# Kernel tuning notes

Measured on AMD Instinct MI355X. Metric: run time of the kernel, lower is better.

The kernel has to match this reference:

```python
import jax, jax.numpy as jnp
import numpy as np

EMBED_DIM = 1024
NUM_HEADS = 16
HEAD_DIM = EMBED_DIM // NUM_HEADS
HIDDEN_DIM = 4096
EPS = 1e-5


def setup_inputs() -> dict:
    key = jax.random.key(0)
    ks = jax.random.split(key, 12)
    B, N, C, H = 4, 2048, EMBED_DIM, HIDDEN_DIM
    s = 0.02
    return {
        "x": jax.random.normal(ks[0], (B, N, C), jnp.float32),
        "ln1_g": jnp.ones((C,), jnp.float32),
        "ln1_b": jnp.zeros((C,), jnp.float32),
        "w_qkv": jax.random.normal(ks[1], (C, 3 * C), jnp.float32) * s,
        "w_proj": jax.random.normal(ks[2], (C, C), jnp.float32) * s,
        "b_proj": jnp.zeros((C,), jnp.float32),
        "ln2_g": jnp.ones((C,), jnp.float32),
        "ln2_b": jnp.zeros((C,), jnp.float32),
        "w1": jax.random.normal(ks[3], (C, H), jnp.float32) * s,
        "b1": jnp.zeros((H,), jnp.float32),
        "w2": jax.random.normal(ks[4], (H, C), jnp.float32) * s,
        "b2": jnp.zeros((C,), jnp.float32),
    }


def _layernorm(x, g, b):
    mu = jnp.mean(x, axis=-1, keepdims=True)
    var = jnp.mean(jnp.square(x - mu), axis=-1, keepdims=True)
    return (x - mu) * jax.lax.rsqrt(var + EPS) * g + b


def reference(x, ln1_g, ln1_b, w_qkv, w_proj, b_proj, ln2_g, ln2_b, w1, b1, w2, b2):
    B, N, C = x.shape
    # --- attention sub-block ---
    h = _layernorm(x, ln1_g, ln1_b)
    qkv = h @ w_qkv  # [B,N,3C]
    qkv = qkv.reshape(B, N, 3, NUM_HEADS, HEAD_DIM).transpose(2, 0, 3, 1, 4)
    q, k, v = qkv[0], qkv[1], qkv[2]  # each [B,H,N,D]
    scale = HEAD_DIM ** -0.5
    attn = jnp.einsum("bhqd,bhkd->bhqk", q, k) * scale  # materialized scores
    attn = jax.nn.softmax(attn, axis=-1)
    o = jnp.einsum("bhqk,bhkd->bhqd", attn, v)
    o = o.transpose(0, 2, 1, 3).reshape(B, N, C)
    x = x + (o @ w_proj + b_proj)
    # --- MLP sub-block ---
    h = _layernorm(x, ln2_g, ln2_b)
    h = jax.nn.gelu(h @ w1 + b1, approximate=False)
    x = x + (h @ w2 + b2)
    return x
```

## Files before the change

kernel.cpp:

```cpp
#include <hip/hip_runtime.h>

#define B_    4
#define SEQ   2048
#define CDIM  1024
#define NHEAD 16
#define HDIM  64
#define HID   4096
#define MTOK  (B_*SEQ)

typedef unsigned short ushort_t;
typedef __bf16 bf16x8 __attribute__((ext_vector_type(8)));
typedef float  floatx4 __attribute__((ext_vector_type(4)));

static __device__ __forceinline__ float us2f(ushort_t u) {
    union { unsigned u; float f; } z; z.u = ((unsigned)u) << 16; return z.f;
}
static __device__ __forceinline__ ushort_t f2us(float f) {
    union { float f; unsigned u; } z; z.f = f;
    unsigned r = z.u + 0x7fffu + ((z.u >> 16) & 1u);
    return (ushort_t)(r >> 16);
}

static __device__ __forceinline__ void gl_lds16(const ushort_t* g, ushort_t* l) {
    __builtin_amdgcn_global_load_lds(
        (const __attribute__((address_space(1))) void*)g,
        (__attribute__((address_space(3))) void*)l,
        16, 0, 0);
}

__global__ void k_detect(const unsigned* __restrict__ g1, int* __restrict__ flagp) {
    if (threadIdx.x == 0) flagp[0] = (g1[0] == 0x3F803F80u) ? 0 : 1;
}

template <typename TIN>
__global__ __launch_bounds__(256) void k_cvt_params(const int* __restrict__ flagp,
        const void* s0, const void* s1, const void* s2, const void* s3,
        const void* s4, const void* s5, const void* s6,
        ushort_t* __restrict__ dst) {
    const int want = (sizeof(TIN) == 2) ? 0 : 1;
    if (*flagp != want) return;
    const int seg = blockIdx.y;
    const int i = blockIdx.x * 256 + threadIdx.x;
    const int sizes[7] = {1024, 1024, 1024, 1024, 1024, 4096, 1024};
    const int offs[7]  = {0, 1024, 2048, 3072, 4096, 5120, 9216};
    const void* sp = seg == 0 ? s0 : seg == 1 ? s1 : seg == 2 ? s2 :
                     seg == 3 ? s3 : seg == 4 ? s4 : seg == 5 ? s5 : s6;
    if (i < sizes[seg]) {
        float v = (sizeof(TIN) == 2) ? us2f(((const ushort_t*)sp)[i])
                                     : ((const float*)sp)[i];
        dst[offs[seg] + i] = f2us(v);
    }
}

template <typename TIN>
__global__ __launch_bounds__(256) void k_transpose_cvt(const int* __restrict__ flagp,
                                                       const TIN* __restrict__ src,
                                                       ushort_t* __restrict__ dst,
                                                       int R, int C) {
    const int want = (sizeof(TIN) == 2) ? 0 : 1;
    if (*flagp != want) return;
    __shared__ ushort_t tile[32][33];
    const int c0 = blockIdx.x * 32, r0 = blockIdx.y * 32;
    const int tx = threadIdx.x & 31, ty = threadIdx.x >> 5;
    #pragma unroll
    for (int i = ty; i < 32; i += 8) {
        TIN v = src[(size_t)(r0 + i) * C + c0 + tx];
        if constexpr (sizeof(TIN) == 2) tile[i][tx] = (ushort_t)v;
        else                            tile[i][tx] = f2us((float)v);
    }
    __syncthreads();
    #pragma unroll
    for (int i = ty; i < 32; i += 8)
        dst[(size_t)(c0 + i) * R + r0 + tx] = tile[tx][i];
}

template <int SRC>
__global__ __launch_bounds__(256) void k_layernorm(const int* __restrict__ flagp,
                                                   const float* __restrict__ xf,
                                                   const ushort_t* __restrict__ xb,
                                                   const ushort_t* __restrict__ gam,
                                                   const ushort_t* __restrict__ bet,
                                                   ushort_t* __restrict__ out) {
    const int row = blockIdx.x, t = threadIdx.x;
    const int lane = t & 63, wv = t >> 6;
    const size_t base = (size_t)row * CDIM + t * 4;
    float v[4];
    if (SRC == 1 || *flagp != 0) {
        float4 f = *(const float4*)(xf + base);
        v[0] = f.x; v[1] = f.y; v[2] = f.z; v[3] = f.w;
    } else {
        ushort4 u = *(const ushort4*)(xb + base);
        v[0] = us2f(u.x); v[1] = us2f(u.y); v[2] = us2f(u.z); v[3] = us2f(u.w);
    }
    float s = v[0] + v[1] + v[2] + v[3];
    float s2 = v[0]*v[0] + v[1]*v[1] + v[2]*v[2] + v[3]*v[3];
    #pragma unroll
    for (int m = 1; m < 64; m <<= 1) {
        s  += __shfl_xor(s,  m, 64);
        s2 += __shfl_xor(s2, m, 64);
    }
    __shared__ float redbuf[8];
    if (lane == 0) { redbuf[wv] = s; redbuf[4 + wv] = s2; }
    __syncthreads();
    s  = redbuf[0] + redbuf[1] + redbuf[2] + redbuf[3];
    s2 = redbuf[4] + redbuf[5] + redbuf[6] + redbuf[7];
    const float mu  = s * (1.0f / CDIM);
    const float var = s2 * (1.0f / CDIM) - mu * mu;
    const float rstd = rsqrtf(var + 1e-5f);
    const int cb = t * 4;
    ushort4 o;
    o.x = f2us((v[0] - mu) * rstd * us2f(gam[cb + 0]) + us2f(bet[cb + 0]));
    o.y = f2us((v[1] - mu) * rstd * us2f(gam[cb + 1]) + us2f(bet[cb + 1]));
    o.z = f2us((v[2] - mu) * rstd * us2f(gam[cb + 2]) + us2f(bet[cb + 2]));
    o.w = f2us((v[3] - mu) * rstd * us2f(gam[cb + 3]) + us2f(bet[cb + 3]));
    *(ushort4*)(out + base) = o;
}

enum { EPI_STORE_BF16 = 0, EPI_BIAS_RES_F32 = 1, EPI_BIAS_GELU_BF16 = 2, EPI_FINAL = 3 };

template <int EPI>
__global__ __launch_bounds__(256) void k_gemm_bt(const ushort_t* __restrict__ A,
                                                 const ushort_t* __restrict__ Bt,
                                                 const ushort_t* __restrict__ bias,
                                                 const float* __restrict__ resF,
                                                 const ushort_t* __restrict__ resU,
                                                 float* __restrict__ outF,
                                                 ushort_t* __restrict__ outB,
                                                 const int* __restrict__ flagp,
                                                 int M, int N, int K) {
    __shared__ ushort_t As[128 * 64];
    __shared__ ushort_t Bs[128 * 64];
    const int t = threadIdx.x, lane = t & 63, wv = t >> 6;
    const int quad = lane >> 4, cc = lane & 15;
    const int wm = wv >> 1, wn = wv & 1;
    const int m0 = blockIdx.y * 128, n0 = blockIdx.x * 128;

    floatx4 zv = {0.f, 0.f, 0.f, 0.f};
    floatx4 acc[4][4];
    #pragma unroll
    for (int a = 0; a < 4; a++)
        #pragma unroll
        for (int b = 0; b < 4; b++) acc[a][b] = zv;

    for (int k0 = 0; k0 < K; k0 += 64) {
        #pragma unroll
        for (int i = 0; i < 4; i++) {
            const int L = i * 256 + t;
            const int row = L >> 3;
            const int kc = (L & 7) ^ (row & 7);
            gl_lds16(A  + (size_t)(m0 + row) * K + k0 + kc * 8,
                     As + (size_t)(i * 256 + wv * 64) * 8);
            gl_lds16(Bt + (size_t)(n0 + row) * K + k0 + kc * 8,
                     Bs + (size_t)(i * 256 + wv * 64) * 8);
        }
        __syncthreads();
        #pragma unroll
        for (int ks = 0; ks < 2; ks++) {
            const int ph = ((ks * 4 + quad) ^ (cc & 7)) * 8;
            bf16x8 af[4], bfr[4];
            #pragma unroll
            for (int x = 0; x < 4; x++) {
                af[x]  = *(const bf16x8*)(As + (size_t)(wm * 64 + x * 16 + cc) * 64 + ph);
                bfr[x] = *(const bf16x8*)(Bs + (size_t)(wn * 64 + x * 16 + cc) * 64 + ph);
            }
            #pragma unroll
            for (int tm = 0; tm < 4; tm++)
                #pragma unroll
                for (int tn = 0; tn < 4; tn++)
                    acc[tm][tn] = __builtin_amdgcn_mfma_f32_16x16x32_bf16(
                        af[tm], bfr[tn], acc[tm][tn], 0, 0, 0);
        }
        __syncthreads();
    }

    int flag = 0;
    if (EPI == EPI_BIAS_RES_F32 || EPI == EPI_FINAL) flag = *flagp;

    #pragma unroll
    for (int tm = 0; tm < 4; tm++) {
        #pragma unroll
        for (int tn = 0; tn < 4; tn++) {
            const int col = n0 + wn * 64 + tn * 16 + cc;
            const float bv = (EPI != EPI_STORE_BF16) ? us2f(bias[col]) : 0.f;
            #pragma unroll
            for (int i = 0; i < 4; i++) {
                const int row = m0 + wm * 64 + tm * 16 + quad * 4 + i;
                const size_t idx = (size_t)row * N + col;
                float v = acc[tm][tn][i] + bv;
                if (EPI == EPI_STORE_BF16) {
                    outB[idx] = f2us(v);
                } else if (EPI == EPI_BIAS_RES_F32) {
                    outF[idx] = v + (flag ? resF[idx] : us2f(resU[idx]));
                } else if (EPI == EPI_BIAS_GELU_BF16) {
                    float g = 0.5f * v * (1.0f + erff(v * 0.70710678f));
                    outB[idx] = f2us(g);
                } else {
                    float w = v + resF[idx];
                    if (flag != 0) outF[idx] = w;
                    else           outB[idx] = f2us(w);
                }
            }
        }
    }
}

__global__ __launch_bounds__(256) void k_attention(const ushort_t* __restrict__ qkv,
                                                   ushort_t* __restrict__ o) {
    __shared__ ushort_t Kc[64 * 64];
    __shared__ unsigned Vt[64][32];
    __shared__ ushort_t Ps[4][32][72];

    const int qt = blockIdx.x, h = blockIdx.y, b = blockIdx.z;
    const int t = threadIdx.x, lane = t & 63, wv = t >> 6;
    const int quad = lane >> 4, cc = lane & 15;
    const size_t rstr = 3 * CDIM;
    const ushort_t* Qb = qkv + (size_t)b * SEQ * rstr + h * HDIM;
    const ushort_t* Kb = Qb + CDIM;
    const ushort_t* Vb = Qb + 2 * CDIM;

    const float qscale = 0.125f * 1.44269504f;
    bf16x8 aq[2][2];
    #pragma unroll
    for (int mt = 0; mt < 2; mt++) {
        const int qrow = qt * 128 + wv * 32 + mt * 16 + cc;
        #pragma unroll
        for (int ks = 0; ks < 2; ks++) {
            bf16x8 r = *(const bf16x8*)(Qb + (size_t)qrow * rstr + ks * 32 + quad * 8);
            #pragma unroll
            for (int j = 0; j < 8; j++) r[j] = (__bf16)((float)r[j] * qscale);
            aq[mt][ks] = r;
        }
    }

    floatx4 zv = {0.f, 0.f, 0.f, 0.f};
    floatx4 oacc[2][4];
    #pragma unroll
    for (int mt = 0; mt < 2; mt++)
        #pragma unroll
        for (int dg = 0; dg < 4; dg++) oacc[mt][dg] = zv;
    float lacc[2][4];
    #pragma unroll
    for (int mt = 0; mt < 2; mt++)
        #pragma unroll
        for (int i = 0; i < 4; i++) lacc[mt][i] = 0.f;

    const int kp = t >> 3, dseg = t & 7;

    for (int k0 = 0; k0 < SEQ; k0 += 64) {
        #pragma unroll
        for (int ii = 0; ii < 2; ii++) {
            const int L = ii * 256 + t;
            const int key = L >> 3;
            const int kc = (L & 7) ^ (key & 7);
            gl_lds16(Kb + (size_t)(k0 + key) * rstr + kc * 8,
                     Kc + (size_t)(ii * 256 + wv * 64) * 8);
        }
        {
            const ushort_t* vp0 = Vb + (size_t)(k0 + 2 * kp) * rstr + dseg * 8;
            const ushort_t* vp1 = vp0 + rstr;
            ushort4 a0 = *(const ushort4*)(vp0);
            ushort4 a1 = *(const ushort4*)(vp0 + 4);
            ushort4 b0 = *(const ushort4*)(vp1);
            ushort4 b1 = *(const ushort4*)(vp1 + 4);
            ushort_t u0[8] = {a0.x, a0.y, a0.z, a0.w, a1.x, a1.y, a1.z, a1.w};
            ushort_t u1[8] = {b0.x, b0.y, b0.z, b0.w, b1.x, b1.y, b1.z, b1.w};
            #pragma unroll
            for (int jj = 0; jj < 8; jj++) {
                int d = dseg * 8 + jj;
                unsigned val = (unsigned)u0[jj] | ((unsigned)u1[jj] << 16);
                int phys = (kp >> 2) ^ jj ^ dseg;
                Vt[d][phys * 4 + (kp & 3)] = val;
            }
        }
        __syncthreads();

        floatx4 s[2][4];
        #pragma unroll
        for (int mt = 0; mt < 2; mt++)
            #pragma unroll
            for (int g = 0; g < 4; g++) s[mt][g] = zv;
        #pragma unroll
        for (int g = 0; g < 4; g++) {
            const int ph0 = (quad ^ (cc & 7)) * 8;
            const int ph1 = ((4 + quad) ^ (cc & 7)) * 8;
            bf16x8 bk0 = *(const bf16x8*)(Kc + (size_t)(g * 16 + cc) * 64 + ph0);
            bf16x8 bk1 = *(const bf16x8*)(Kc + (size_t)(g * 16 + cc) * 64 + ph1);
            #pragma unroll
            for (int mt = 0; mt < 2; mt++) {
                s[mt][g] = __builtin_amdgcn_mfma_f32_16x16x32_bf16(aq[mt][0], bk0, s[mt][g], 0, 0, 0);
                s[mt][g] = __builtin_amdgcn_mfma_f32_16x16x32_bf16(aq[mt][1], bk1, s[mt][g], 0, 0, 0);
            }
        }

        #pragma unroll
        for (int mt = 0; mt < 2; mt++)
            #pragma unroll
            for (int g = 0; g < 4; g++)
                #pragma unroll
                for (int i = 0; i < 4; i++) {
                    float p = __builtin_amdgcn_exp2f(s[mt][g][i]);
                    lacc[mt][i] += p;
                    Ps[wv][mt * 16 + quad * 4 + i][g * 16 + cc] = f2us(p);
                }

        #pragma unroll
        for (int ks = 0; ks < 2; ks++) {
            bf16x8 bv[4];
            #pragma unroll
            for (int dg = 0; dg < 4; dg++) {
                int d = dg * 16 + cc;
                int phys = (ks * 4 + quad) ^ (d & 7) ^ (d >> 3);
                bv[dg] = *(const bf16x8*)(&Vt[d][phys * 4]);
            }
            #pragma unroll
            for (int mt = 0; mt < 2; mt++) {
                bf16x8 ap = *(const bf16x8*)(&Ps[wv][mt * 16 + cc][ks * 32 + quad * 8]);
                #pragma unroll
                for (int dg = 0; dg < 4; dg++)
                    oacc[mt][dg] = __builtin_amdgcn_mfma_f32_16x16x32_bf16(ap, bv[dg], oacc[mt][dg], 0, 0, 0);
            }
        }
        __syncthreads();
    }

    #pragma unroll
    for (int m = 1; m < 16; m <<= 1)
        #pragma unroll
        for (int mt = 0; mt < 2; mt++)
            #pragma unroll
            for (int i = 0; i < 4; i++)
                lacc[mt][i] += __shfl_xor(lacc[mt][i], m, 64);

    #pragma unroll
    for (int mt = 0; mt < 2; mt++) {
        float rl[4];
        #pragma unroll
        for (int i = 0; i < 4; i++) rl[i] = __frcp_rn(lacc[mt][i]);
        #pragma unroll
        for (int dg = 0; dg < 4; dg++)
            #pragma unroll
            for (int i = 0; i < 4; i++) {
                const int row = qt * 128 + wv * 32 + mt * 16 + quad * 4 + i;
                o[(size_t)(b * SEQ + row) * CDIM + h * HDIM + dg * 16 + cc] =
                    f2us(oacc[mt][dg][i] * rl[i]);
            }
    }
}

extern "C" void kernel_launch(void* const* d_in, const int* in_sizes, int n_in,
                              void* d_out, int out_size, void* d_ws, size_t ws_size,
                              hipStream_t stream) {
    const void* x     = d_in[0];
    const void* ln1g  = d_in[1];
    const void* ln1b  = d_in[2];
    const void* wqkv  = d_in[3];
    const void* wproj = d_in[4];
    const void* bproj = d_in[5];
    const void* ln2g  = d_in[6];
    const void* ln2b  = d_in[7];
    const void* w1    = d_in[8];
    const void* b1    = d_in[9];
    const void* w2    = d_in[10];
    const void* b2    = d_in[11];

    char* ws = (char*)d_ws;
    size_t off = 0;
    auto alloc = [&](size_t bytes) {
        void* p = ws + off;
        off += (bytes + 255) & ~(size_t)255;
        return p;
    };
    int*      flagp  = (int*)alloc(256);
    ushort_t* params = (ushort_t*)alloc((size_t)10240 * 2);
    ushort_t* wqkvT  = (ushort_t*)alloc((size_t)3072 * 1024 * 2);
    ushort_t* wprojT = (ushort_t*)alloc((size_t)1024 * 1024 * 2);
    ushort_t* w1T    = (ushort_t*)alloc((size_t)4096 * 1024 * 2);
    ushort_t* w2T    = (ushort_t*)alloc((size_t)1024 * 4096 * 2);
    float*    x1     = (float*)alloc((size_t)MTOK * CDIM * 4);
    ushort_t* bufA   = (ushort_t*)alloc((size_t)MTOK * HID * 2);
    ushort_t* bufB   = (ushort_t*)alloc((size_t)MTOK * 3 * CDIM * 2);

    ushort_t* p_ln1g = params + 0;
    ushort_t* p_ln1b = params + 1024;
    ushort_t* p_ln2g = params + 2048;
    ushort_t* p_ln2b = params + 3072;
    ushort_t* p_bprj = params + 4096;
    ushort_t* p_b1   = params + 5120;
    ushort_t* p_b2   = params + 9216;

    ushort_t* h   = bufA;
    ushort_t* qkv = bufB;
    ushort_t* oo  = bufA;
    ushort_t* h2  = bufB;
    ushort_t* hh  = bufA;

    k_detect<<<1, 64, 0, stream>>>((const unsigned*)ln1g, flagp);
    k_cvt_params<ushort_t><<<dim3(16, 7), 256, 0, stream>>>(flagp,
        ln1g, ln1b, ln2g, ln2b, bproj, b1, b2, params);
    k_cvt_params<float><<<dim3(16, 7), 256, 0, stream>>>(flagp,
        ln1g, ln1b, ln2g, ln2b, bproj, b1, b2, params);
    k_transpose_cvt<ushort_t><<<dim3(96, 32),  256, 0, stream>>>(flagp, (const ushort_t*)wqkv,  wqkvT,  1024, 3072);
    k_transpose_cvt<float   ><<<dim3(96, 32),  256, 0, stream>>>(flagp, (const float*)wqkv,     wqkvT,  1024, 3072);
    k_transpose_cvt<ushort_t><<<dim3(32, 32),  256, 0, stream>>>(flagp, (const ushort_t*)wproj, wprojT, 1024, 1024);
    k_transpose_cvt<float   ><<<dim3(32, 32),  256, 0, stream>>>(flagp, (const float*)wproj,    wprojT, 1024, 1024);
    k_transpose_cvt<ushort_t><<<dim3(128, 32), 256, 0, stream>>>(flagp, (const ushort_t*)w1,    w1T,    1024, 4096);
    k_transpose_cvt<float   ><<<dim3(128, 32), 256, 0, stream>>>(flagp, (const float*)w1,       w1T,    1024, 4096);
    k_transpose_cvt<ushort_t><<<dim3(32, 128), 256, 0, stream>>>(flagp, (const ushort_t*)w2,    w2T,    4096, 1024);
    k_transpose_cvt<float   ><<<dim3(32, 128), 256, 0, stream>>>(flagp, (const float*)w2,       w2T,    4096, 1024);

    k_layernorm<0><<<MTOK, 256, 0, stream>>>(flagp, (const float*)x, (const ushort_t*)x, p_ln1g, p_ln1b, h);
    k_gemm_bt<EPI_STORE_BF16><<<dim3(24, 64), 256, 0, stream>>>(
        h, wqkvT, nullptr, nullptr, nullptr, nullptr, qkv, flagp, MTOK, 3072, 1024);
    k_attention<<<dim3(SEQ / 128, NHEAD, B_), 256, 0, stream>>>(qkv, oo);
    k_gemm_bt<EPI_BIAS_RES_F32><<<dim3(8, 64), 256, 0, stream>>>(
        oo, wprojT, p_bprj, (const float*)x, (const ushort_t*)x, x1, nullptr, flagp, MTOK, 1024, 1024);
    k_layernorm<1><<<MTOK, 256, 0, stream>>>(flagp, x1, nullptr, p_ln2g, p_ln2b, h2);
    k_gemm_bt<EPI_BIAS_GELU_BF16><<<dim3(32, 64), 256, 0, stream>>>(
        h2, w1T, p_b1, nullptr, nullptr, nullptr, hh, flagp, MTOK, 4096, 1024);
    k_gemm_bt<EPI_FINAL><<<dim3(8, 64), 256, 0, stream>>>(
        hh, w2T, p_b2, x1, nullptr, (float*)d_out, (ushort_t*)d_out, flagp, MTOK, 1024, 4096);
}
```

Before: 598.6 us.

## Emit transposed V and prescaled Q from QKV GEMM, double-buffer attention, merge prep kernels

The QKV GEMM epilogue now folds the softmax scale into Q and writes V in a per-head transposed layout to a new buffer. Attention can then load both K and V into LDS with async global-to-LDS copies, double-buffered, with one barrier per chunk instead of two. The grid is reordered so blocks of the same head run together. The exact erf GELU is replaced by a tanh-style exp2/rcp approximation, the final normalisation uses a fast reciprocal, and the duplicated dtype-specialised weight transpose and parameter conversion launches are merged into single runtime-flag kernels. The changes add an extra V buffer and reduce GELU accuracy.

```diff
diff --git a/kernel.cpp b/kernel.cpp
--- a/kernel.cpp
+++ b/kernel.cpp
@@ -32,13 +32,11 @@
     if (threadIdx.x == 0) flagp[0] = (g1[0] == 0x3F803F80u) ? 0 : 1;
 }
 
-template <typename TIN>
 __global__ __launch_bounds__(256) void k_cvt_params(const int* __restrict__ flagp,
         const void* s0, const void* s1, const void* s2, const void* s3,
         const void* s4, const void* s5, const void* s6,
         ushort_t* __restrict__ dst) {
-    const int want = (sizeof(TIN) == 2) ? 0 : 1;
-    if (*flagp != want) return;
+    const int flag = *flagp;
     const int seg = blockIdx.y;
     const int i = blockIdx.x * 256 + threadIdx.x;
     const int sizes[7] = {1024, 1024, 1024, 1024, 1024, 4096, 1024};
@@ -46,32 +44,35 @@
     const void* sp = seg == 0 ? s0 : seg == 1 ? s1 : seg == 2 ? s2 :
                      seg == 3 ? s3 : seg == 4 ? s4 : seg == 5 ? s5 : s6;
     if (i < sizes[seg]) {
-        float v = (sizeof(TIN) == 2) ? us2f(((const ushort_t*)sp)[i])
-                                     : ((const float*)sp)[i];
+        float v = flag ? ((const float*)sp)[i] : us2f(((const ushort_t*)sp)[i]);
         dst[offs[seg] + i] = f2us(v);
     }
 }
 
-template <typename TIN>
-__global__ __launch_bounds__(256) void k_transpose_cvt(const int* __restrict__ flagp,
-                                                       const TIN* __restrict__ src,
-                                                       ushort_t* __restrict__ dst,
-                                                       int R, int C) {
-    const int want = (sizeof(TIN) == 2) ? 0 : 1;
-    if (*flagp != want) return;
-    __shared__ ushort_t tile[32][33];
-    const int c0 = blockIdx.x * 32, r0 = blockIdx.y * 32;
+__global__ __launch_bounds__(256) void k_transpose_all(const int* __restrict__ flagp,
+        const void* s_qkv, const void* s_proj, const void* s_w1, const void* s_w2,
+        ushort_t* __restrict__ d_qkv, ushort_t* __restrict__ d_proj,
+        ushort_t* __restrict__ d_w1, ushort_t* __restrict__ d_w2) {
+    const int id = blockIdx.x;
+    const void* src; ushort_t* dst; int R, C, tile;
+    if (id < 3072)      { src = s_qkv;  dst = d_qkv;  R = 1024; C = 3072; tile = id; }
+    else if (id < 4096) { src = s_proj; dst = d_proj; R = 1024; C = 1024; tile = id - 3072; }
+    else if (id < 8192) { src = s_w1;   dst = d_w1;   R = 1024; C = 4096; tile = id - 4096; }
+    else                { src = s_w2;   dst = d_w2;   R = 4096; C = 1024; tile = id - 8192; }
+    const int ct = C >> 5;
+    const int c0 = (tile % ct) * 32, r0 = (tile / ct) * 32;
+    const int flag = *flagp;
+    __shared__ ushort_t tl[32][33];
     const int tx = threadIdx.x & 31, ty = threadIdx.x >> 5;
     #pragma unroll
     for (int i = ty; i < 32; i += 8) {
-        TIN v = src[(size_t)(r0 + i) * C + c0 + tx];
-        if constexpr (sizeof(TIN) == 2) tile[i][tx] = (ushort_t)v;
-        else                            tile[i][tx] = f2us((float)v);
+        const size_t gi = (size_t)(r0 + i) * C + c0 + tx;
+        tl[i][tx] = flag ? f2us(((const float*)src)[gi]) : ((const ushort_t*)src)[gi];
     }
     __syncthreads();
     #pragma unroll
     for (int i = ty; i < 32; i += 8)
-        dst[(size_t)(c0 + i) * R + r0 + tx] = tile[tx][i];
+        dst[(size_t)(c0 + i) * R + r0 + tx] = tl[tx][i];
 }
 
 template <int SRC>
@@ -116,7 +117,7 @@
     *(ushort4*)(out + base) = o;
 }
 
-enum { EPI_STORE_BF16 = 0, EPI_BIAS_RES_F32 = 1, EPI_BIAS_GELU_BF16 = 2, EPI_FINAL = 3 };
+enum { EPI_QKV = 0, EPI_BIAS_RES_F32 = 1, EPI_BIAS_GELU_BF16 = 2, EPI_FINAL = 3 };
 
 template <int EPI>
 __global__ __launch_bounds__(256) void k_gemm_bt(const ushort_t* __restrict__ A,
@@ -126,6 +127,7 @@
                                                  const ushort_t* __restrict__ resU,
                                                  float* __restrict__ outF,
                                                  ushort_t* __restrict__ outB,
+                                                 ushort_t* __restrict__ outV,
                                                  const int* __restrict__ flagp,
                                                  int M, int N, int K) {
     __shared__ ushort_t As[128 * 64];
@@ -181,55 +183,73 @@
         #pragma unroll
         for (int tn = 0; tn < 4; tn++) {
             const int col = n0 + wn * 64 + tn * 16 + cc;
-            const float bv = (EPI != EPI_STORE_BF16) ? us2f(bias[col]) : 0.f;
-            #pragma unroll
-            for (int i = 0; i < 4; i++) {
-                const int row = m0 + wm * 64 + tm * 16 + quad * 4 + i;
-                const size_t idx = (size_t)row * N + col;
-                float v = acc[tm][tn][i] + bv;
-                if (EPI == EPI_STORE_BF16) {
-                    outB[idx] = f2us(v);
-                } else if (EPI == EPI_BIAS_RES_F32) {
-                    outF[idx] = v + (flag ? resF[idx] : us2f(resU[idx]));
-                } else if (EPI == EPI_BIAS_GELU_BF16) {
-                    float g = 0.5f * v * (1.0f + erff(v * 0.70710678f));
-                    outB[idx] = f2us(g);
+            if (EPI == EPI_QKV) {
+                if (col < 2048) {
+                    const float sc = (col < 1024) ? 0.125f * 1.44269504f : 1.0f;
+                    #pragma unroll
+                    for (int i = 0; i < 4; i++) {
+                        const int row = m0 + wm * 64 + tm * 16 + quad * 4 + i;
+                        outB[(size_t)row * 3072 + col] = f2us(acc[tm][tn][i] * sc);
+                    }
                 } else {
-                    float w = v + resF[idx];
-                    if (flag != 0) outF[idx] = w;
-                    else           outB[idx] = f2us(w);
+                    const int hh = (col - 2048) >> 6, d = (col - 2048) & 63;
+                    const int r0w = m0 + wm * 64 + tm * 16 + quad * 4;
+                    const int bh = (r0w >> 11) * NHEAD + hh;
+                    const int np = r0w & (SEQ - 1);
+                    ushort4 pk;
+                    pk.x = f2us(acc[tm][tn][0]);
+                    pk.y = f2us(acc[tm][tn][1]);
+                    pk.z = f2us(acc[tm][tn][2]);
+                    pk.w = f2us(acc[tm][tn][3]);
+                    *(ushort4*)(outV + ((size_t)bh * 64 + d) * SEQ + np) = pk;
                 }
+            } else {
+                const float bv = us2f(bias[col]);
+                #pragma unroll
+                for (int i = 0; i < 4; i++) {
+                    const int row = m0 + wm * 64 + tm * 16 + quad * 4 + i;
+                    const size_t idx = (size_t)row * N + col;
+                    float v = acc[tm][tn][i] + bv;
+                    if (EPI == EPI_BIAS_RES_F32) {
+                        outF[idx] = v + (flag ? resF[idx] : us2f(resU[idx]));
+                    } else if (EPI == EPI_BIAS_GELU_BF16) {
+                        float u = v * v;
+                        float w = -2.3022134f * v * __builtin_fmaf(0.044715f, u, 1.0f);
+                        float e = __builtin_amdgcn_exp2f(fminf(w, 126.0f));
+                        outB[idx] = f2us(v * __builtin_amdgcn_rcpf(1.0f + e));
+                    } else {
+                        float w = v + resF[idx];
+                        if (flag != 0) outF[idx] = w;
+                        else           outB[idx] = f2us(w);
+                    }
+                }
             }
         }
     }
 }
 
 __global__ __launch_bounds__(256) void k_attention(const ushort_t* __restrict__ qkv,
+                                                   const ushort_t* __restrict__ vT,
                                                    ushort_t* __restrict__ o) {
-    __shared__ ushort_t Kc[64 * 64];
-    __shared__ unsigned Vt[64][32];
+    __shared__ ushort_t Kc[2][64 * 64];
+    __shared__ ushort_t Vt[2][64 * 64];
     __shared__ ushort_t Ps[4][32][72];
 
-    const int qt = blockIdx.x, h = blockIdx.y, b = blockIdx.z;
+    const int bh = blockIdx.x, qt = blockIdx.y;
+    const int b = bh >> 4, h = bh & 15;
     const int t = threadIdx.x, lane = t & 63, wv = t >> 6;
     const int quad = lane >> 4, cc = lane & 15;
     const size_t rstr = 3 * CDIM;
     const ushort_t* Qb = qkv + (size_t)b * SEQ * rstr + h * HDIM;
     const ushort_t* Kb = Qb + CDIM;
-    const ushort_t* Vb = Qb + 2 * CDIM;
-
-    const float qscale = 0.125f * 1.44269504f;
+    const ushort_t* Vb = vT + (size_t)bh * HDIM * SEQ;
+
     bf16x8 aq[2][2];
     #pragma unroll
     for (int mt = 0; mt < 2; mt++) {
         const int qrow = qt * 128 + wv * 32 + mt * 16 + cc;
-        #pragma unroll
-        for (int ks = 0; ks < 2; ks++) {
-            bf16x8 r = *(const bf16x8*)(Qb + (size_t)qrow * rstr + ks * 32 + quad * 8);
-            #pragma unroll
-            for (int j = 0; j < 8; j++) r[j] = (__bf16)((float)r[j] * qscale);
-            aq[mt][ks] = r;
-        }
+        aq[mt][0] = *(const bf16x8*)(Qb + (size_t)qrow * rstr + quad * 8);
+        aq[mt][1] = *(const bf16x8*)(Qb + (size_t)qrow * rstr + 32 + quad * 8);
     }
 
     floatx4 zv = {0.f, 0.f, 0.f, 0.f};
@@ -244,35 +264,27 @@
         #pragma unroll
         for (int i = 0; i < 4; i++) lacc[mt][i] = 0.f;
 
-    const int kp = t >> 3, dseg = t & 7;
-
-    for (int k0 = 0; k0 < SEQ; k0 += 64) {
+    auto stage = [&](int c, int buf) {
+        const int k0 = c * 64;
         #pragma unroll
         for (int ii = 0; ii < 2; ii++) {
             const int L = ii * 256 + t;
             const int key = L >> 3;
-            const int kc = (L & 7) ^ (key & 7);
-            gl_lds16(Kb + (size_t)(k0 + key) * rstr + kc * 8,
-                     Kc + (size_t)(ii * 256 + wv * 64) * 8);
-        }
-        {
-            const ushort_t* vp0 = Vb + (size_t)(k0 + 2 * kp) * rstr + dseg * 8;
-            const ushort_t* vp1 = vp0 + rstr;
-            ushort4 a0 = *(const ushort4*)(vp0);
-            ushort4 a1 = *(const ushort4*)(vp0 + 4);
-            ushort4 b0 = *(const ushort4*)(vp1);
-            ushort4 b1 = *(const ushort4*)(vp1 + 4);
-            ushort_t u0[8] = {a0.x, a0.y, a0.z, a0.w, a1.x, a1.y, a1.z, a1.w};
-            ushort_t u1[8] = {b0.x, b0.y, b0.z, b0.w, b1.x, b1.y, b1.z, b1.w};
-            #pragma unroll
-            for (int jj = 0; jj < 8; jj++) {
-                int d = dseg * 8 + jj;
-                unsigned val = (unsigned)u0[jj] | ((unsigned)u1[jj] << 16);
-                int phys = (kp >> 2) ^ jj ^ dseg;
-                Vt[d][phys * 4 + (kp & 3)] = val;
-            }
-        }
+            const int kck = (L & 7) ^ (key & 7);
+            gl_lds16(Kb + (size_t)(k0 + key) * rstr + kck * 8,
+                     &Kc[buf][(size_t)(ii * 256 + wv * 64) * 8]);
+            const int kcv = (L & 7) ^ (key & 7);
+            gl_lds16(Vb + (size_t)key * SEQ + k0 + kcv * 8,
+                     &Vt[buf][(size_t)(ii * 256 + wv * 64) * 8]);
+        }
+    };
+
+    stage(0, 0);
+
+    for (int c = 0; c < SEQ / 64; c++) {
         __syncthreads();
+        if (c + 1 < SEQ / 64) stage(c + 1, (c + 1) & 1);
+        const int bf = c & 1;
 
         floatx4 s[2][4];
         #pragma unroll
@@ -281,10 +293,9 @@
             for (int g = 0; g < 4; g++) s[mt][g] = zv;
         #pragma unroll
         for (int g = 0; g < 4; g++) {
-            const int ph0 = (quad ^ (cc & 7)) * 8;
-            const int ph1 = ((4 + quad) ^ (cc & 7)) * 8;
-            bf16x8 bk0 = *(const bf16x8*)(Kc + (size_t)(g * 16 + cc) * 64 + ph0);
-            bf16x8 bk1 = *(const bf16x8*)(Kc + (size_t)(g * 16 + cc) * 64 + ph1);
+            const ushort_t* kr = &Kc[bf][(size_t)(g * 16 + cc) * 64];
+            bf16x8 bk0 = *(const bf16x8*)(kr + (quad ^ (cc & 7)) * 8);
+            bf16x8 bk1 = *(const bf16x8*)(kr + ((4 + quad) ^ (cc & 7)) * 8);
             #pragma unroll
             for (int mt = 0; mt < 2; mt++) {
                 s[mt][g] = __builtin_amdgcn_mfma_f32_16x16x32_bf16(aq[mt][0], bk0, s[mt][g], 0, 0, 0);
@@ -308,9 +319,9 @@
             bf16x8 bv[4];
             #pragma unroll
             for (int dg = 0; dg < 4; dg++) {
-                int d = dg * 16 + cc;
-                int phys = (ks * 4 + quad) ^ (d & 7) ^ (d >> 3);
-                bv[dg] = *(const bf16x8*)(&Vt[d][phys * 4]);
+                const int d = dg * 16 + cc;
+                const int phys = ((ks * 4 + quad) ^ (cc & 7)) * 8;
+                bv[dg] = *(const bf16x8*)(&Vt[bf][(size_t)d * 64 + phys]);
             }
             #pragma unroll
             for (int mt = 0; mt < 2; mt++) {
@@ -320,7 +331,6 @@
                     oacc[mt][dg] = __builtin_amdgcn_mfma_f32_16x16x32_bf16(ap, bv[dg], oacc[mt][dg], 0, 0, 0);
             }
         }
-        __syncthreads();
     }
 
     #pragma unroll
@@ -335,7 +345,7 @@
     for (int mt = 0; mt < 2; mt++) {
         float rl[4];
         #pragma unroll
-        for (int i = 0; i < 4; i++) rl[i] = __frcp_rn(lacc[mt][i]);
+        for (int i = 0; i < 4; i++) rl[i] = __builtin_amdgcn_rcpf(lacc[mt][i]);
         #pragma unroll
         for (int dg = 0; dg < 4; dg++)
             #pragma unroll
@@ -376,6 +386,7 @@
     ushort_t* wprojT = (ushort_t*)alloc((size_t)1024 * 1024 * 2);
     ushort_t* w1T    = (ushort_t*)alloc((size_t)4096 * 1024 * 2);
     ushort_t* w2T    = (ushort_t*)alloc((size_t)1024 * 4096 * 2);
+    ushort_t* vTb    = (ushort_t*)alloc((size_t)MTOK * CDIM * 2);
     float*    x1     = (float*)alloc((size_t)MTOK * CDIM * 4);
     ushort_t* bufA   = (ushort_t*)alloc((size_t)MTOK * HID * 2);
     ushort_t* bufB   = (ushort_t*)alloc((size_t)MTOK * 3 * CDIM * 2);
@@ -395,28 +406,20 @@
     ushort_t* hh  = bufA;
 
     k_detect<<<1, 64, 0, stream>>>((const unsigned*)ln1g, flagp);
-    k_cvt_params<ushort_t><<<dim3(16, 7), 256, 0, stream>>>(flagp,
+    k_cvt_params<<<dim3(16, 7), 256, 0, stream>>>(flagp,
         ln1g, ln1b, ln2g, ln2b, bproj, b1, b2, params);
-    k_cvt_params<float><<<dim3(16, 7), 256, 0, stream>>>(flagp,
-        ln1g, ln1b, ln2g, ln2b, bproj, b1, b2, params);
-    k_transpose_cvt<ushort_t><<<dim3(96, 32),  256, 0, stream>>>(flagp, (const ushort_t*)wqkv,  wqkvT,  1024, 3072);
-    k_transpose_cvt<float   ><<<dim3(96, 32),  256, 0, stream>>>(flagp, (const float*)wqkv,     wqkvT,  1024, 3072);
-    k_transpose_cvt<ushort_t><<<dim3(32, 32),  256, 0, stream>>>(flagp, (const ushort_t*)wproj, wprojT, 1024, 1024);
-    k_transpose_cvt<float   ><<<dim3(32, 32),  256, 0, stream>>>(flagp, (const float*)wproj,    wprojT, 1024, 1024);
-    k_transpose_cvt<ushort_t><<<dim3(128, 32), 256, 0, stream>>>(flagp, (const ushort_t*)w1,    w1T,    1024, 4096);
-    k_transpose_cvt<float   ><<<dim3(128, 32), 256, 0, stream>>>(flagp, (const float*)w1,       w1T,    1024, 4096);
-    k_transpose_cvt<ushort_t><<<dim3(32, 128), 256, 0, stream>>>(flagp, (const ushort_t*)w2,    w2T,    4096, 1024);
-    k_transpose_cvt<float   ><<<dim3(32, 128), 256, 0, stream>>>(flagp, (const float*)w2,       w2T,    4096, 1024);
+    k_transpose_all<<<12288, 256, 0, stream>>>(flagp,
+        wqkv, wproj, w1, w2, wqkvT, wprojT, w1T, w2T);
 
     k_layernorm<0><<<MTOK, 256, 0, stream>>>(flagp, (const float*)x, (const ushort_t*)x, p_ln1g, p_ln1b, h);
-    k_gemm_bt<EPI_STORE_BF16><<<dim3(24, 64), 256, 0, stream>>>(
-        h, wqkvT, nullptr, nullptr, nullptr, nullptr, qkv, flagp, MTOK, 3072, 1024);
-    k_attention<<<dim3(SEQ / 128, NHEAD, B_), 256, 0, stream>>>(qkv, oo);
+    k_gemm_bt<EPI_QKV><<<dim3(24, 64), 256, 0, stream>>>(
+        h, wqkvT, nullptr, nullptr, nullptr, nullptr, qkv, vTb, flagp, MTOK, 3072, 1024);
+    k_attention<<<dim3(B_ * NHEAD, SEQ / 128), 256, 0, stream>>>(qkv, vTb, oo);
     k_gemm_bt<EPI_BIAS_RES_F32><<<dim3(8, 64), 256, 0, stream>>>(
-        oo, wprojT, p_bprj, (const float*)x, (const ushort_t*)x, x1, nullptr, flagp, MTOK, 1024, 1024);
+        oo, wprojT, p_bprj, (const float*)x, (const ushort_t*)x, x1, nullptr, nullptr, flagp, MTOK, 1024, 1024);
     k_layernorm<1><<<MTOK, 256, 0, stream>>>(flagp, x1, nullptr, p_ln2g, p_ln2b, h2);
     k_gemm_bt<EPI_BIAS_GELU_BF16><<<dim3(32, 64), 256, 0, stream>>>(
-        h2, w1T, p_b1, nullptr, nullptr, nullptr, hh, flagp, MTOK, 4096, 1024);
+        h2, w1T, p_b1, nullptr, nullptr, nullptr, hh, nullptr, flagp, MTOK, 4096, 1024);
     k_gemm_bt<EPI_FINAL><<<dim3(8, 64), 256, 0, stream>>>(
-        hh, w2T, p_b2, x1, nullptr, (float*)d_out, (ushort_t*)d_out, flagp, MTOK, 1024, 4096);
-}
+        hh, w2T, p_b2, x1, nullptr, (float*)d_out, (ushort_t*)d_out, nullptr, flagp, MTOK, 1024, 4096);
+}
```

Result: faster. 565.3 us (-5.6%).
